# Performance work log

Hardware: AMD Instinct MI355X
Metric: run time of the kernel (lower is better)

Reference implementation:

```python
import jax, jax.numpy as jnp
import numpy as np

B, V, K = 128, 128000, 20
_SAMPLING_EPS = 1e-5


def setup_inputs() -> dict:
    key = jax.random.key(0)
    k1, k2, k3 = jax.random.split(key, 3)
    logits = jax.random.normal(k1, (B, V), dtype=jnp.float32)
    temp = jax.random.uniform(k2, (B,), dtype=jnp.float32, minval=0.2, maxval=1.5)
    # every 4th sequence is greedy (temperature < eps)
    temp = jnp.where(jnp.arange(B) % 4 == 0, 0.0, temp)
    # uniform noise in (0,1); exponential noise is q = -log(u)
    u = jax.random.uniform(k3, (B, V), dtype=jnp.float32, minval=1e-7, maxval=1.0)
    return {"logits": logits, "temp": temp, "u": u, "max_num_logprobs": K}


def reference(logits, temp, u, max_num_logprobs):
    # apply_temperature: greedy rows (temp < eps) use temp=1.0
    t = jnp.where(temp < _SAMPLING_EPS, 1.0, temp)
    scaled = logits.astype(jnp.float32) / t[:, None]          # [B, V]
    probs = jax.nn.softmax(scaled, axis=-1)                    # [B, V]
    # greedy sample
    greedy = jnp.argmax(probs, axis=1)                         # [B]
    # random sample via exponential-race (Gumbel-max equivalent): argmax(probs / Exp(1))
    q = -jnp.log(u)                                            # Exp(1) noise
    random_sampled = jnp.argmax(probs / q, axis=1)             # [B]
    sampled = jnp.where(temp < _SAMPLING_EPS, greedy, random_sampled)
    # top-k logprobs
    logprobs = jax.nn.log_softmax(scaled, axis=-1)             # [B, V]
    topk_logprobs, topk_indices = jax.lax.top_k(logprobs, max_num_logprobs)
    return sampled, topk_logprobs, topk_indices
```

## Files before the change

### kernel.cpp

```cpp
#include <hip/hip_runtime.h>
#include <stdint.h>


#define KMAX 20
#define SAMPLING_EPS 1e-5f
#define TAU 3.0f
#define CPB 64

static __device__ __forceinline__ unsigned int ord32(float v) {
    unsigned int u = __float_as_uint(v);
    return u ^ ((unsigned int)((int)u >> 31) | 0x80000000u);
}
static __device__ __forceinline__ float unord32(unsigned int x) {
    unsigned int u = (x & 0x80000000u) ? (x ^ 0x80000000u) : ~x;
    return __uint_as_float(u);
}
static __device__ __forceinline__ unsigned long long shflxor64(unsigned long long v, int off) {
    int lo = __shfl_xor((int)(unsigned int)v, off, 64);
    int hi = __shfl_xor((int)(unsigned int)(v >> 32), off, 64);
    return ((unsigned long long)(unsigned int)hi << 32) | (unsigned int)lo;
}

static __device__ __forceinline__ float gumbel_exact(float x, float inv_t, float uu, float wm) {
    const float q = (uu > 0.984375f) ? -log1pf(-wm) : -__logf(uu);
    return x * inv_t - __logf(q);
}

__global__ __launch_bounds__(256, 8) void k1_partials(
        const float* __restrict__ logits, const float* __restrict__ u,
        const float* __restrict__ temp,
        unsigned int* __restrict__ wrec,
        unsigned int* __restrict__ cntbuf,
        uint2* __restrict__ candbuf,
        int V, int nsplit) {
    __shared__ int cnt;
    __shared__ uint2 cand[CPB];
    const int b = blockIdx.x;
    const int r = b / nsplit;
    const int sp = b - r * nsplit;
    const int t = threadIdx.x;
    const int lane = t & 63;
    const int w = t >> 6;
    if (t == 0) cnt = 0;
    __syncthreads();

    const float traw = temp[r];
    const bool greedy = traw < SAMPLING_EPS;
    const float inv_t = greedy ? 1.0f : (1.0f / traw);

    const int nf4 = V >> 2;
    const int per = (nf4 + nsplit - 1) / nsplit;
    const int f0 = sp * per;
    const int f1 = min(f0 + per, nf4);

    const float4* __restrict__ l4 = (const float4*)(logits + (size_t)r * V);
    const float4* __restrict__ u4 = (const float4*)(u + (size_t)r * V);

    float s = 0.0f;
    float gv = -INFINITY;
    int gcol = 0;

    if (greedy) {
        for (int f = f0 + t; f < f1; f += 256) {
            const float4 lv = l4[f];
            const int colb = f << 2;
            #pragma unroll
            for (int j = 0; j < 4; ++j) {
                const float x = (&lv.x)[j];
                s += __expf(x * inv_t);
                if (x >= TAU) {
                    const int idx = atomicAdd(&cnt, 1);
                    if (idx < CPB) cand[idx] = make_uint2(__float_as_uint(x), (unsigned)(colb + j));
                }
            }
        }
    } else {
        int f = f0 + t;
        if (f < f1) {
            const float4 lv = l4[f];
            const float4 uv = u4[f];
            const int colb = f << 2;
            #pragma unroll
            for (int j = 0; j < 4; ++j) {
                const float x = (&lv.x)[j];
                s += __expf(x * inv_t);
                const float uu = (&uv.x)[j];
                const float g = gumbel_exact(x, inv_t, uu, 1.0f - uu);
                if (g > gv) { gv = g; gcol = colb + j; }
                if (x >= TAU) {
                    const int idx = atomicAdd(&cnt, 1);
                    if (idx < CPB) cand[idx] = make_uint2(__float_as_uint(x), (unsigned)(colb + j));
                }
            }
        }
        float gmax = gv;
        #pragma unroll
        for (int off = 1; off < 64; off <<= 1) gmax = fmaxf(gmax, __shfl_xor(gmax, off, 64));
        float gvs = gmax - 1e-5f;

        for (f += 256; f < f1; f += 256) {
            const float4 lv = l4[f];
            const float4 uv = u4[f];
            const int colb = f << 2;
            #pragma unroll
            for (int j = 0; j < 4; ++j) {
                const float x = (&lv.x)[j];
                const float arg = x * inv_t;
                s += __expf(arg);
                const float uu = (&uv.x)[j];
                const float wm = 1.0f - uu;
                const int ew = 127 - (int)(__float_as_uint(wm) >> 23);
                const float gub = fmaf((float)ew, 0.69314718f, arg);
                if (gub > gvs) {
                    const float g = gumbel_exact(x, inv_t, uu, wm);
                    if (g > gv) { gv = g; gcol = colb + j; gvs = g - 1e-5f; }
                }
                if (x >= TAU) {
                    const int idx = atomicAdd(&cnt, 1);
                    if (idx < CPB) cand[idx] = make_uint2(__float_as_uint(x), (unsigned)(colb + j));
                }
            }
        }
    }

    #pragma unroll
    for (int off = 1; off < 64; off <<= 1) s += __shfl_xor(s, off, 64);
    unsigned long long gk = greedy ? 0ull
        : (((unsigned long long)ord32(gv) << 32) | (unsigned int)~(unsigned int)gcol);
    #pragma unroll
    for (int off = 1; off < 64; off <<= 1) {
        const unsigned long long o = shflxor64(gk, off);
        gk = (o > gk) ? o : gk;
    }
    if (lane == 0) {
        unsigned int* rp = wrec + (size_t)(b * 4 + w) * 4;
        rp[0] = __float_as_uint(s);
        rp[1] = __float_as_uint(unord32((unsigned int)(gk >> 32)));
        rp[2] = ~(unsigned int)gk;
    }
    __syncthreads();
    const int c = cnt;
    if (t == 0) cntbuf[b] = (unsigned)c;
    if (t < min(c, CPB)) candbuf[(size_t)b * CPB + t] = cand[t];
}

__global__ __launch_bounds__(64) void k2_finalize(
        const unsigned int* __restrict__ wrec, const unsigned int* __restrict__ cntbuf,
        const uint2* __restrict__ candbuf, const float* __restrict__ logits,
        const float* __restrict__ temp, float* __restrict__ out,
        int B, int V, int K, int nsplit) {
    __shared__ unsigned long long kbuf[512];
    const int r = blockIdx.x;
    const int lane = threadIdx.x;
    const int NW = nsplit * 4;

    const float traw = temp[r];
    const bool greedy = traw < SAMPLING_EPS;
    const float tt = greedy ? 1.0f : traw;

    float s = 0.0f;
    unsigned long long gk = 0ull;
    if (lane < NW) {
        const unsigned int* rp = wrec + (size_t)(r * NW + lane) * 4;
        s = __uint_as_float(rp[0]);
        gk = ((unsigned long long)ord32(__uint_as_float(rp[1])) << 32) | (unsigned int)~rp[2];
    }
    #pragma unroll
    for (int off = 1; off < 64; off <<= 1) s += __shfl_xor(s, off, 64);
    #pragma unroll
    for (int off = 1; off < 64; off <<= 1) {
        const unsigned long long o = shflxor64(gk, off);
        gk = (o > gk) ? o : gk;
    }
    const float lS = logf(s);

    const int cnt_raw = (lane < nsplit) ? (int)cntbuf[r * nsplit + lane] : 0;
    const int cntc = min(cnt_raw, CPB);
    const bool ovf = __ballot(cnt_raw > CPB) != 0ull;
    int incl = cntc;
    #pragma unroll
    for (int d = 1; d < 64; d <<= 1) {
        const int o = __shfl_up(incl, d, 64);
        if (lane >= d) incl += o;
    }
    const int T = __shfl(incl, 63, 64);
    const int off0 = incl - cntc;

    unsigned long long keys[8];
    #pragma unroll
    for (int jj = 0; jj < 8; ++jj) keys[jj] = 0ull;

    if (!ovf && T >= K && T <= 512) {
        if (lane < nsplit) {
            const uint2* cb = candbuf + (size_t)(r * nsplit + lane) * CPB;
            for (int i = 0; i < cntc; ++i) {
                const uint2 e = cb[i];
                kbuf[off0 + i] = ((unsigned long long)ord32(__uint_as_float(e.x)) << 32)
                               | (unsigned int)~e.y;
            }
        }
        __syncthreads();
        #pragma unroll
        for (int jj = 0; jj < 8; ++jj) {
            const int idx = lane + 64 * jj;
            if (idx < T) keys[jj] = kbuf[idx];
        }
    } else {
        unsigned long long mykey = ((unsigned long long)0x007FFFFFu) << 32;
        unsigned long long minkey = mykey;
        float vmin = -INFINITY;
        const float* lr = logits + (size_t)r * V;
        for (int base = 0; base < V; base += 64) {
            const int i = base + lane;
            const float x = (i < V) ? lr[i] : -INFINITY;
            unsigned long long cm = __ballot((i < V) && (x >= vmin));
            while (cm) {
                const int src = (int)__builtin_ctzll(cm);
                cm &= cm - 1;
                const float cv = __shfl(x, src, 64);
                const int cc = __shfl(i, src, 64);
                const unsigned long long ck =
                    ((unsigned long long)ord32(cv) << 32) | (unsigned int)~(unsigned int)cc;
                if (ck > minkey) {
                    const bool own = (lane < K) && (mykey == minkey);
                    const unsigned long long om = __ballot(own);
                    if (lane == (int)__builtin_ctzll(om)) mykey = ck;
                    unsigned long long mk = (lane < K) ? mykey : ~0ull;
                    #pragma unroll
                    for (int o2 = 1; o2 < 64; o2 <<= 1) {
                        const unsigned long long o = shflxor64(mk, o2);
                        mk = (o < mk) ? o : mk;
                    }
                    minkey = mk;
                    vmin = unord32((unsigned int)(mk >> 32));
                }
            }
        }
        keys[0] = (lane < K) ? mykey : 0ull;
    }

    float* out_s  = out;
    float* out_lp = out + B;
    float* out_ix = out + B + (size_t)B * K;

    unsigned int top1 = 0;
    for (int k = 0; k < K; ++k) {
        unsigned long long loc = keys[0];
        #pragma unroll
        for (int jj = 1; jj < 8; ++jj) loc = (keys[jj] > loc) ? keys[jj] : loc;
        #pragma unroll
        for (int off = 1; off < 64; off <<= 1) {
            const unsigned long long o = shflxor64(loc, off);
            loc = (o > loc) ? o : loc;
        }
        #pragma unroll
        for (int jj = 0; jj < 8; ++jj) if (keys[jj] == loc) keys[jj] = 0ull;
        if (lane == 0) {
            const unsigned int col = ~(unsigned int)loc;
            const float v = unord32((unsigned int)(loc >> 32));
            out_lp[(size_t)r * K + k] = v / tt - lS;
            out_ix[(size_t)r * K + k] = (float)col;
            if (k == 0) top1 = col;
        }
    }
    if (lane == 0) {
        out_s[r] = (float)(greedy ? top1 : (~(unsigned int)gk));
    }
}

extern "C" void kernel_launch(void* const* d_in, const int* in_sizes, int n_in,
                              void* d_out, int out_size, void* d_ws, size_t ws_size,
                              hipStream_t stream) {
    const float* logits = (const float*)d_in[0];
    const float* temp   = (const float*)d_in[1];
    const float* u      = (const float*)d_in[2];
    const int B = in_sizes[1];
    const int V = in_sizes[0] / B;
    int K = (out_size - B) / (2 * B);
    if (K > KMAX) K = KMAX;
    if (K < 1) K = 1;

    int nsplit = 16;
    while (nsplit > 1 && (size_t)B * nsplit * 580 > ws_size) nsplit >>= 1;
    const int blocks = B * nsplit;

    unsigned int* wrec   = (unsigned int*)d_ws;
    unsigned int* cntbuf = wrec + (size_t)blocks * 16;
    uint2*        candbf = (uint2*)(cntbuf + blocks);

    k1_partials<<<dim3(blocks), dim3(256), 0, stream>>>(
        logits, u, temp, wrec, cntbuf, candbf, V, nsplit);
    k2_finalize<<<dim3(B), dim3(64), 0, stream>>>(
        wrec, cntbuf, candbf, logits, temp, (float*)d_out, B, V, K, nsplit);
}
```

Measured before the change: 163.5 us.

## Unroll k1 loads by two, use exp2, cheaper Gumbel bound, and remap block-to-row order

The partials kernel now processes two float4s per iteration with four independent sum accumulators, uses hardware exp2 with a prescaled inverse temperature, and computes the Gumbel upper bound in log2 domain from the raw float bits, checking a vectorized max before the exact per-element path. Candidate pushes are gated by a max over the loaded values. Blocks are remapped to rows via a permutation so that concurrently running blocks spread across different rows (and memory channels), with output slots keyed by row and split. Occupancy hint drops from 8 to 6 waves per SIMD, and the looser bound margin may trigger more exact evaluations.

```diff
diff --git a/kernel.cpp b/kernel.cpp
--- a/kernel.cpp
+++ b/kernel.cpp
@@ -6,6 +6,16 @@
 #define SAMPLING_EPS 1e-5f
 #define TAU 3.0f
 #define CPB 64
+#define LOG2E 1.44269504f
+#define SMARGIN 3e-4f
+
+static __device__ __forceinline__ float fexp2(float x) {
+#if __has_builtin(__builtin_amdgcn_exp2f)
+    return __builtin_amdgcn_exp2f(x);
+#else
+    return exp2f(x);
+#endif
+}
 
 static __device__ __forceinline__ unsigned int ord32(float v) {
     unsigned int u = __float_as_uint(v);
@@ -26,7 +36,11 @@
     return x * inv_t - __logf(q);
 }
 
-__global__ __launch_bounds__(256, 8) void k1_partials(
+static __device__ __forceinline__ float gub_bound(float a, float uu) {
+    return fmaf((float)__float_as_uint(1.0f - uu), -0x1p-23f, 127.0f + a);
+}
+
+__global__ __launch_bounds__(256, 6) void k1_partials(
         const float* __restrict__ logits, const float* __restrict__ u,
         const float* __restrict__ temp,
         unsigned int* __restrict__ wrec,
@@ -36,17 +50,23 @@
     __shared__ int cnt;
     __shared__ uint2 cand[CPB];
     const int b = blockIdx.x;
-    const int r = b / nsplit;
-    const int sp = b - r * nsplit;
     const int t = threadIdx.x;
     const int lane = t & 63;
     const int w = t >> 6;
     if (t == 0) cnt = 0;
     __syncthreads();
 
+    const int nrows = gridDim.x / nsplit;
+    const int mb = b % nrows;
+    const int sp = b / nrows;
+    int r = (mb * 61 + (sp >> 1)) % nrows;
+    if ((nrows & (nrows - 1)) == 0) r ^= (r >> 4);
+    const int slot = r * nsplit + sp;
+
     const float traw = temp[r];
     const bool greedy = traw < SAMPLING_EPS;
     const float inv_t = greedy ? 1.0f : (1.0f / traw);
+    const float it2 = inv_t * LOG2E;
 
     const int nf4 = V >> 2;
     const int per = (nf4 + nsplit - 1) / nsplit;
@@ -56,73 +76,156 @@
     const float4* __restrict__ l4 = (const float4*)(logits + (size_t)r * V);
     const float4* __restrict__ u4 = (const float4*)(u + (size_t)r * V);
 
-    float s = 0.0f;
+    float s0 = 0.0f, s1 = 0.0f, s2 = 0.0f, s3 = 0.0f;
     float gv = -INFINITY;
     int gcol = 0;
 
+#define PUSH(xv, cc) do { \
+        const int pi_ = atomicAdd(&cnt, 1); \
+        if (pi_ < CPB) cand[pi_] = make_uint2(__float_as_uint(xv), (unsigned)(cc)); \
+    } while (0)
+
     if (greedy) {
-        for (int f = f0 + t; f < f1; f += 256) {
-            const float4 lv = l4[f];
-            const int colb = f << 2;
-            #pragma unroll
-            for (int j = 0; j < 4; ++j) {
-                const float x = (&lv.x)[j];
-                s += __expf(x * inv_t);
-                if (x >= TAU) {
-                    const int idx = atomicAdd(&cnt, 1);
-                    if (idx < CPB) cand[idx] = make_uint2(__float_as_uint(x), (unsigned)(colb + j));
-                }
+        int f = f0 + t;
+        for (; f + 256 < f1; f += 512) {
+            const float4 la = l4[f];
+            const float4 lb = l4[f + 256];
+            s0 += fexp2(la.x * it2); s1 += fexp2(la.y * it2);
+            s2 += fexp2(la.z * it2); s3 += fexp2(la.w * it2);
+            s0 += fexp2(lb.x * it2); s1 += fexp2(lb.y * it2);
+            s2 += fexp2(lb.z * it2); s3 += fexp2(lb.w * it2);
+            const float xm = fmaxf(fmaxf(fmaxf(la.x, la.y), fmaxf(la.z, la.w)),
+                                   fmaxf(fmaxf(lb.x, lb.y), fmaxf(lb.z, lb.w)));
+            if (xm >= TAU) {
+                const int c0 = f << 2, c1 = (f + 256) << 2;
+                if (la.x >= TAU) PUSH(la.x, c0);
+                if (la.y >= TAU) PUSH(la.y, c0 + 1);
+                if (la.z >= TAU) PUSH(la.z, c0 + 2);
+                if (la.w >= TAU) PUSH(la.w, c0 + 3);
+                if (lb.x >= TAU) PUSH(lb.x, c1);
+                if (lb.y >= TAU) PUSH(lb.y, c1 + 1);
+                if (lb.z >= TAU) PUSH(lb.z, c1 + 2);
+                if (lb.w >= TAU) PUSH(lb.w, c1 + 3);
+            }
+        }
+        for (; f < f1; f += 256) {
+            const float4 la = l4[f];
+            s0 += fexp2(la.x * it2); s1 += fexp2(la.y * it2);
+            s2 += fexp2(la.z * it2); s3 += fexp2(la.w * it2);
+            const float xm = fmaxf(fmaxf(la.x, la.y), fmaxf(la.z, la.w));
+            if (xm >= TAU) {
+                const int c0 = f << 2;
+                if (la.x >= TAU) PUSH(la.x, c0);
+                if (la.y >= TAU) PUSH(la.y, c0 + 1);
+                if (la.z >= TAU) PUSH(la.z, c0 + 2);
+                if (la.w >= TAU) PUSH(la.w, c0 + 3);
             }
         }
     } else {
         int f = f0 + t;
         if (f < f1) {
-            const float4 lv = l4[f];
-            const float4 uv = u4[f];
-            const int colb = f << 2;
-            #pragma unroll
-            for (int j = 0; j < 4; ++j) {
-                const float x = (&lv.x)[j];
-                s += __expf(x * inv_t);
-                const float uu = (&uv.x)[j];
-                const float g = gumbel_exact(x, inv_t, uu, 1.0f - uu);
-                if (g > gv) { gv = g; gcol = colb + j; }
-                if (x >= TAU) {
-                    const int idx = atomicAdd(&cnt, 1);
-                    if (idx < CPB) cand[idx] = make_uint2(__float_as_uint(x), (unsigned)(colb + j));
-                }
+            const float4 la = l4[f];
+            const float4 ua = u4[f];
+            const int c0 = f << 2;
+            s0 += fexp2(la.x * it2); s1 += fexp2(la.y * it2);
+            s2 += fexp2(la.z * it2); s3 += fexp2(la.w * it2);
+            { const float g = gumbel_exact(la.x, inv_t, ua.x, 1.0f - ua.x);
+              if (g > gv) { gv = g; gcol = c0; } }
+            { const float g = gumbel_exact(la.y, inv_t, ua.y, 1.0f - ua.y);
+              if (g > gv) { gv = g; gcol = c0 + 1; } }
+            { const float g = gumbel_exact(la.z, inv_t, ua.z, 1.0f - ua.z);
+              if (g > gv) { gv = g; gcol = c0 + 2; } }
+            { const float g = gumbel_exact(la.w, inv_t, ua.w, 1.0f - ua.w);
+              if (g > gv) { gv = g; gcol = c0 + 3; } }
+            const float xm = fmaxf(fmaxf(la.x, la.y), fmaxf(la.z, la.w));
+            if (xm >= TAU) {
+                if (la.x >= TAU) PUSH(la.x, c0);
+                if (la.y >= TAU) PUSH(la.y, c0 + 1);
+                if (la.z >= TAU) PUSH(la.z, c0 + 2);
+                if (la.w >= TAU) PUSH(la.w, c0 + 3);
             }
         }
         float gmax = gv;
         #pragma unroll
         for (int off = 1; off < 64; off <<= 1) gmax = fmaxf(gmax, __shfl_xor(gmax, off, 64));
-        float gvs = gmax - 1e-5f;
-
-        for (f += 256; f < f1; f += 256) {
-            const float4 lv = l4[f];
-            const float4 uv = u4[f];
-            const int colb = f << 2;
-            #pragma unroll
-            for (int j = 0; j < 4; ++j) {
-                const float x = (&lv.x)[j];
-                const float arg = x * inv_t;
-                s += __expf(arg);
-                const float uu = (&uv.x)[j];
-                const float wm = 1.0f - uu;
-                const int ew = 127 - (int)(__float_as_uint(wm) >> 23);
-                const float gub = fmaf((float)ew, 0.69314718f, arg);
-                if (gub > gvs) {
-                    const float g = gumbel_exact(x, inv_t, uu, wm);
-                    if (g > gv) { gv = g; gcol = colb + j; gvs = g - 1e-5f; }
-                }
-                if (x >= TAU) {
-                    const int idx = atomicAdd(&cnt, 1);
-                    if (idx < CPB) cand[idx] = make_uint2(__float_as_uint(x), (unsigned)(colb + j));
-                }
-            }
-        }
-    }
-
+        float gvs2 = fmaf(gmax, LOG2E, -SMARGIN);
+
+#define EX(gj, xv, uu, cc) \
+        if ((gj) > gvs2) { \
+            const float wm_ = 1.0f - (uu); \
+            const float ge_ = gumbel_exact(xv, inv_t, uu, wm_); \
+            if (ge_ > gv) { gv = ge_; gcol = (cc); gvs2 = fmaf(ge_, LOG2E, -SMARGIN); } \
+        }
+
+        for (f += 256; f + 256 < f1; f += 512) {
+            const float4 la = l4[f];
+            const float4 lb = l4[f + 256];
+            const float4 ua = u4[f];
+            const float4 ub = u4[f + 256];
+            const float a0 = la.x * it2, a1 = la.y * it2, a2 = la.z * it2, a3 = la.w * it2;
+            const float a4 = lb.x * it2, a5 = lb.y * it2, a6 = lb.z * it2, a7 = lb.w * it2;
+            s0 += fexp2(a0); s1 += fexp2(a1); s2 += fexp2(a2); s3 += fexp2(a3);
+            s0 += fexp2(a4); s1 += fexp2(a5); s2 += fexp2(a6); s3 += fexp2(a7);
+            const float g0 = gub_bound(a0, ua.x), g1 = gub_bound(a1, ua.y);
+            const float g2 = gub_bound(a2, ua.z), g3 = gub_bound(a3, ua.w);
+            const float g4 = gub_bound(a4, ub.x), g5 = gub_bound(a5, ub.y);
+            const float g6 = gub_bound(a6, ub.z), g7 = gub_bound(a7, ub.w);
+            const float gm = fmaxf(fmaxf(fmaxf(g0, g1), fmaxf(g2, g3)),
+                                   fmaxf(fmaxf(g4, g5), fmaxf(g6, g7)));
+            if (gm > gvs2) {
+                const int c0 = f << 2, c1 = (f + 256) << 2;
+                EX(g0, la.x, ua.x, c0)
+                EX(g1, la.y, ua.y, c0 + 1)
+                EX(g2, la.z, ua.z, c0 + 2)
+                EX(g3, la.w, ua.w, c0 + 3)
+                EX(g4, lb.x, ub.x, c1)
+                EX(g5, lb.y, ub.y, c1 + 1)
+                EX(g6, lb.z, ub.z, c1 + 2)
+                EX(g7, lb.w, ub.w, c1 + 3)
+            }
+            const float xm = fmaxf(fmaxf(fmaxf(la.x, la.y), fmaxf(la.z, la.w)),
+                                   fmaxf(fmaxf(lb.x, lb.y), fmaxf(lb.z, lb.w)));
+            if (xm >= TAU) {
+                const int c0 = f << 2, c1 = (f + 256) << 2;
+                if (la.x >= TAU) PUSH(la.x, c0);
+                if (la.y >= TAU) PUSH(la.y, c0 + 1);
+                if (la.z >= TAU) PUSH(la.z, c0 + 2);
+                if (la.w >= TAU) PUSH(la.w, c0 + 3);
+                if (lb.x >= TAU) PUSH(lb.x, c1);
+                if (lb.y >= TAU) PUSH(lb.y, c1 + 1);
+                if (lb.z >= TAU) PUSH(lb.z, c1 + 2);
+                if (lb.w >= TAU) PUSH(lb.w, c1 + 3);
+            }
+        }
+        for (; f < f1; f += 256) {
+            const float4 la = l4[f];
+            const float4 ua = u4[f];
+            const float a0 = la.x * it2, a1 = la.y * it2, a2 = la.z * it2, a3 = la.w * it2;
+            s0 += fexp2(a0); s1 += fexp2(a1); s2 += fexp2(a2); s3 += fexp2(a3);
+            const float g0 = gub_bound(a0, ua.x), g1 = gub_bound(a1, ua.y);
+            const float g2 = gub_bound(a2, ua.z), g3 = gub_bound(a3, ua.w);
+            const float gm = fmaxf(fmaxf(g0, g1), fmaxf(g2, g3));
+            if (gm > gvs2) {
+                const int c0 = f << 2;
+                EX(g0, la.x, ua.x, c0)
+                EX(g1, la.y, ua.y, c0 + 1)
+                EX(g2, la.z, ua.z, c0 + 2)
+                EX(g3, la.w, ua.w, c0 + 3)
+            }
+            const float xm = fmaxf(fmaxf(la.x, la.y), fmaxf(la.z, la.w));
+            if (xm >= TAU) {
+                const int c0 = f << 2;
+                if (la.x >= TAU) PUSH(la.x, c0);
+                if (la.y >= TAU) PUSH(la.y, c0 + 1);
+                if (la.z >= TAU) PUSH(la.z, c0 + 2);
+                if (la.w >= TAU) PUSH(la.w, c0 + 3);
+            }
+        }
+#undef EX
+    }
+#undef PUSH
+
+    float s = (s0 + s1) + (s2 + s3);
     #pragma unroll
     for (int off = 1; off < 64; off <<= 1) s += __shfl_xor(s, off, 64);
     unsigned long long gk = greedy ? 0ull
@@ -133,15 +236,15 @@
         gk = (o > gk) ? o : gk;
     }
     if (lane == 0) {
-        unsigned int* rp = wrec + (size_t)(b * 4 + w) * 4;
+        unsigned int* rp = wrec + (size_t)(slot * 4 + w) * 4;
         rp[0] = __float_as_uint(s);
         rp[1] = __float_as_uint(unord32((unsigned int)(gk >> 32)));
         rp[2] = ~(unsigned int)gk;
     }
     __syncthreads();
     const int c = cnt;
-    if (t == 0) cntbuf[b] = (unsigned)c;
-    if (t < min(c, CPB)) candbuf[(size_t)b * CPB + t] = cand[t];
+    if (t == 0) cntbuf[slot] = (unsigned)c;
+    if (t < min(c, CPB)) candbuf[(size_t)slot * CPB + t] = cand[t];
 }
 
 __global__ __launch_bounds__(64) void k2_finalize(
```

Result: faster. 159.7 us (-2.3%).
